# Performance work log

Measured on AMD Instinct MI355X. Metric: run time of the kernel, lower is better.

## Reference

```python
import jax, jax.numpy as jnp
import numpy as np

HEADS = 8
KSIZE = 3


def _unfold(t, ksize):
    # t: [B, C, H, W] -> [B, C, k*k, H, W], zero padding k//2, stride 1
    B, C, H, W = t.shape
    pad = ksize // 2
    tp = jnp.pad(t, ((0, 0), (0, 0), (pad, pad), (pad, pad)))
    patches = [tp[:, :, i:i + H, j:j + W] for i in range(ksize) for j in range(ksize)]
    return jnp.stack(patches, axis=2)


def setup_inputs() -> dict:
    key = jax.random.key(0)
    k0, k1, k2, k3 = jax.random.split(key, 4)
    B, C, H, W = 2, 256, 96, 96
    x = jax.random.normal(k0, (B, C, H, W), dtype=jnp.float32)
    w_qkv = jax.random.normal(k1, (3 * C, C), dtype=jnp.float32) * 0.02  # 1x1 conv, no bias
    w_out = jax.random.normal(k2, (C, C), dtype=jnp.float32) * 0.02     # 1x1 conv
    b_out = jax.random.normal(k3, (C,), dtype=jnp.float32) * 0.02
    return {"x": x, "w_qkv": w_qkv, "w_out": w_out, "b_out": b_out}


def reference(x, w_qkv, w_out, b_out):
    B, C, H, W = x.shape
    hd = C // HEADS
    scale = hd ** (-0.5)
    kk = KSIZE * KSIZE

    qkv = jnp.einsum('bchw,oc->bohw', x, w_qkv)          # [B, 3C, H, W]
    q, k, v = jnp.split(qkv, 3, axis=1)
    # unfold -> [B, heads, C/heads, k^2, H, W]
    q, k, v = [_unfold(t, KSIZE).reshape(B, HEADS, hd, kk, H, W) for t in (q, k, v)]

    # contract over the k^2 window dim (s); n,m are the per-head channel dims
    dots = jnp.einsum('bhnsij,bhmsij->bhnmij', q * scale, k)  # [B,h,hd,hd,H,W]
    attn = jax.nn.softmax(dots, axis=3)                       # softmax over m (dim=-3)
    out = jnp.einsum('bhnmij,bhmsij->bhnsij', attn, v)        # [B,h,hd,k^2,H,W]
    out = out.reshape(B, C, kk, H, W).sum(axis=2)             # [B,C,H,W]
    out = jnp.einsum('bchw,oc->bohw', out, w_out) + b_out[None, :, None, None] + x
    return out
```

## Files before the change

### kernel.cpp

```cpp
#include <hip/hip_runtime.h>

#define H96 96
#define W96 96
#define HW  9216
#define NC  256
#define NB  2
#define NHEADS 8
#define HD  32
#define SCALE 0.17677669529663687f

typedef __attribute__((ext_vector_type(8))) short short8v;
typedef __attribute__((ext_vector_type(4))) float f32x4;
typedef __attribute__((ext_vector_type(16))) float f32x16;

__device__ __forceinline__ ushort f2bf(float f) {
    unsigned u = __float_as_uint(f);
    u += 0x7FFFu + ((u >> 16) & 1u);
    return (ushort)(u >> 16);
}
__device__ __forceinline__ float bf2f(ushort h) {
    return __uint_as_float(((unsigned)h) << 16);
}

__global__ __launch_bounds__(256)
void x_to_bf16t(const float* __restrict__ x, ushort* __restrict__ xt,
                ushort* __restrict__ xbm)
{
    __shared__ float tile[32][33];
    const int t = threadIdx.x;
    const int hw0 = blockIdx.x * 32, c0 = blockIdx.y * 32, b = blockIdx.z;

    const int r = t >> 3, cc = (t & 7) * 4;
    const size_t gidx = ((size_t)b * NC + c0 + r) * HW + hw0 + cc;
    const float4 v = *(const float4*)(x + gidx);
    tile[r][cc + 0] = v.x; tile[r][cc + 1] = v.y; tile[r][cc + 2] = v.z; tile[r][cc + 3] = v.w;
    ushort4 ob;
    ob.x = f2bf(v.x); ob.y = f2bf(v.y); ob.z = f2bf(v.z); ob.w = f2bf(v.w);
    *(ushort4*)(xbm + gidx) = ob;
    __syncthreads();

    const int hwr = t >> 3, c4 = (t & 7) * 4;
    ushort4 o;
    o.x = f2bf(tile[c4 + 0][hwr]);
    o.y = f2bf(tile[c4 + 1][hwr]);
    o.z = f2bf(tile[c4 + 2][hwr]);
    o.w = f2bf(tile[c4 + 3][hwr]);
    *(ushort4*)(xt + ((size_t)b * HW + hw0 + hwr) * NC + c0 + c4) = o;
}

__global__ __launch_bounds__(256)
void conv_bf16(const float* __restrict__ w, ushort* __restrict__ o, int nscale)
{
    const int i = (blockIdx.x * 256 + threadIdx.x) * 4;
    const float s = (i < nscale) ? SCALE : 1.0f;
    const float4 v = *(const float4*)(w + i);
    ushort4 u;
    u.x = f2bf(v.x * s); u.y = f2bf(v.y * s); u.z = f2bf(v.z * s); u.w = f2bf(v.w * s);
    *(ushort4*)(o + i) = u;
}

__device__ __forceinline__ void stage_tile(const ushort* __restrict__ g, ushort* lds,
                                           int w, int lane)
{
    const int lr  = lane >> 3;
    const int swz = ((lane & 7) ^ lr) * 8;
    #pragma unroll
    for (int ii = 0; ii < 4; ++ii) {
        const int rowbase = w * 32 + ii * 8;
        const ushort* src = g + (size_t)(rowbase + lr) * NC + swz;
        __builtin_amdgcn_global_load_lds((const __attribute__((address_space(1))) void*)src,
                                         (__attribute__((address_space(3))) void*)(lds + rowbase * 64),
                                         16, 0, 0);
    }
}

template<int EPI>
__global__ __launch_bounds__(256)
void gemm_mfma(const ushort* __restrict__ A, const ushort* __restrict__ Bt,
               void* __restrict__ Cout, const float* __restrict__ bias,
               const ushort* __restrict__ resb, int Mtot)
{
    __shared__ __align__(16) ushort smem[128 * 136];
    ushort* As = smem;
    ushort* Bs = smem + 128 * 64;

    const int t = threadIdx.x;
    const int lane = t & 63, w = t >> 6;
    const int wm = w >> 1, wn = w & 1;
    const int n0 = blockIdx.x * 128;
    const int m0 = blockIdx.y * 128;

    const ushort* Ag = A + (size_t)m0 * NC;
    const ushort* Bg = Bt + (size_t)n0 * NC;

    f32x4 acc[4][4];
    #pragma unroll
    for (int i = 0; i < 4; ++i)
        #pragma unroll
        for (int j = 0; j < 4; ++j)
            acc[i][j] = (f32x4){0.f, 0.f, 0.f, 0.f};

    for (int k0 = 0; k0 < NC; k0 += 64) {
        stage_tile(Ag + k0, As, w, lane);
        stage_tile(Bg + k0, Bs, w, lane);
        __syncthreads();
        #pragma unroll
        for (int ks = 0; ks < 2; ++ks) {
            const int kc = (lane >> 4) + ks * 4;
            const int sw = (kc ^ (lane & 7)) * 8;
            short8v af[4], bf_[4];
            #pragma unroll
            for (int f = 0; f < 4; ++f) {
                af[f]  = *(const short8v*)(As + (wm * 64 + f * 16 + (lane & 15)) * 64 + sw);
                bf_[f] = *(const short8v*)(Bs + (wn * 64 + f * 16 + (lane & 15)) * 64 + sw);
            }
            #pragma unroll
            for (int fi = 0; fi < 4; ++fi)
                #pragma unroll
                for (int fj = 0; fj < 4; ++fj)
                    acc[fi][fj] = __builtin_amdgcn_mfma_f32_16x16x32_bf16(af[fi], bf_[fj], acc[fi][fj], 0, 0, 0);
        }
        __syncthreads();
    }

    const int b = n0 / HW;
    const int hw0 = n0 - b * HW;

    if constexpr (EPI == 0) {
        #pragma unroll
        for (int fi = 0; fi < 4; ++fi)
            #pragma unroll
            for (int fj = 0; fj < 4; ++fj) {
                const int hwl = wn * 64 + fj * 16 + (lane & 15);
                const int ml  = wm * 64 + fi * 16 + (lane >> 4) * 4;
                ushort4 v4;
                v4.x = f2bf(acc[fi][fj][0]);
                v4.y = f2bf(acc[fi][fj][1]);
                v4.z = f2bf(acc[fi][fj][2]);
                v4.w = f2bf(acc[fi][fj][3]);
                *(ushort4*)(smem + hwl * 136 + ml) = v4;
            }
        __syncthreads();
        ushort* C = (ushort*)Cout;
        #pragma unroll
        for (int it = 0; it < 8; ++it) {
            const int cid = it * 256 + t;
            const int hwl = cid >> 4, mc = (cid & 15) * 8;
            const uint4 v = *(const uint4*)(smem + hwl * 136 + mc);
            *(uint4*)(C + ((size_t)b * HW + hw0 + hwl) * (size_t)Mtot + m0 + mc) = v;
        }
    } else {
        float* C = (float*)Cout;
        const int ncol = hw0 + wn * 64 + (lane & 15);
        #pragma unroll
        for (int fi = 0; fi < 4; ++fi)
            #pragma unroll
            for (int r = 0; r < 4; ++r) {
                const int m = m0 + wm * 64 + fi * 16 + (lane >> 4) * 4 + r;
                const float bm = bias[m];
                const size_t base = ((size_t)b * NC + m) * HW + ncol;
                #pragma unroll
                for (int fj = 0; fj < 4; ++fj)
                    C[base + fj * 16] = acc[fi][fj][r] + bm + bf2f(resb[base + fj * 16]);
            }
    }
}

__global__ __launch_bounds__(256)
void attn_mfma(const ushort* __restrict__ qkvp, ushort* __restrict__ att)
{
    __shared__ ushort kh[107 * 40];
    __shared__ ushort qh[72 * 40];
    __shared__ ushort vh[54 * 40];
    __shared__ float  vs[16 * 32];

    const int t = threadIdx.x;
    const int sraw = blockIdx.x;
    const int strip = (sraw & 7) * 72 + (sraw >> 3);
    const int h = blockIdx.y;
    const int b = blockIdx.z;
    const int i0 = strip / 6;
    const int j0 = (strip - (strip / 6) * 6) * 16;

    const ushort* P = qkvp + (size_t)b * HW * 768;
    const int qo = h * HD, ko = NC + h * HD, vo = 2 * NC + h * HD;

    if (t < 216) {
        const int px = t >> 2, c8 = (t & 3) * 8;
        const int dy = px / 18, dx = px - dy * 18;
        const int gi = i0 - 1 + dy, gj = j0 - 1 + dx;
        uint4 qv = {0, 0, 0, 0}, kv = {0, 0, 0, 0}, vv = {0, 0, 0, 0};
        if (gi >= 0 && gi < H96 && gj >= 0 && gj < W96) {
            const ushort* pp = P + ((size_t)gi * W96 + gj) * 768;
            qv = *(const uint4*)(pp + qo + c8);
            kv = *(const uint4*)(pp + ko + c8);
            vv = *(const uint4*)(pp + vo + c8);
        }
        *(uint4*)(qh + px * 40 + c8) = qv;
        *(uint4*)(kh + px * 40 + c8) = kv;
        *(uint4*)(vh + px * 40 + c8) = vv;
    }
    {
        const int u = t;
        #pragma unroll
        for (int pass = 0; pass < 2; ++pass) {
            const int z = u + pass * 256;
            if (z < 265) {
                const int row_id = z / 5, part = z - row_id * 5;
                ushort* dst;
                if (row_id < 18)      dst = kh + (54 + row_id) * 40;
                else if (row_id < 35) dst = kh + (90 + row_id - 18) * 40;
                else                  dst = qh + (54 + row_id - 35) * 40;
                *(uint4*)(dst + part * 8) = (uint4){0, 0, 0, 0};
            }
        }
    }
    __syncthreads();

    {
        const int px = t >> 4, m2 = (t & 15) * 2;
        float a0 = 0.f, a1 = 0.f;
        #pragma unroll
        for (int dy = 0; dy < 3; ++dy)
            #pragma unroll
            for (int dx = 0; dx < 3; ++dx) {
                const ushort* pv = vh + (dy * 18 + px + dx) * 40 + m2;
                a0 += bf2f(pv[0]);
                a1 += bf2f(pv[1]);
            }
        vs[px * 32 + m2]     = a0;
        vs[px * 32 + m2 + 1] = a1;
    }
    __syncthreads();

    const int lane = t & 63, w = t >> 6;
    const int hi = lane >> 5, ch = lane & 31;

    const ushort* kb = kh + (hi * 36 + w * 4) * 40 + ch;
    const ushort* qb = qh + (hi * 36 + w * 4) * 40 + ch;

    #pragma unroll
    for (int p = 0; p < 4; ++p) {
        const int c = w * 4 + p;

        short8v ak, bq;
        #pragma unroll
        for (int e = 0; e < 8; ++e) {
            const int DK[8] = {0, 1, 2, 18, 19, 20, 54, 55};
            const int DQ[8] = {0, 1, 2, 18, 19, 20, 0, 0};
            ak[e] = (short)kb[(p + DK[e]) * 40];
            bq[e] = (short)qb[(p + DQ[e]) * 40];
        }

        f32x16 dm;
        #pragma unroll
        for (int r = 0; r < 16; ++r) dm[r] = 0.f;
        dm = __builtin_amdgcn_mfma_f32_32x32x16_bf16(ak, bq, dm, 0, 0, 0);

        float mx = dm[0];
        #pragma unroll
        for (int r = 1; r < 16; ++r) mx = fmaxf(mx, dm[r]);
        mx = fmaxf(mx, __shfl_xor(mx, 32));

        float vsv[16];
        #pragma unroll
        for (int g = 0; g < 4; ++g) {
            const float4 vv = *(const float4*)(vs + c * 32 + g * 8 + hi * 4);
            vsv[g * 4 + 0] = vv.x; vsv[g * 4 + 1] = vv.y;
            vsv[g * 4 + 2] = vv.z; vsv[g * 4 + 3] = vv.w;
        }

        float sum = 0.f, out = 0.f;
        #pragma unroll
        for (int r = 0; r < 16; ++r) {
            const float pe = __expf(dm[r] - mx);
            sum += pe;
            out = fmaf(pe, vsv[r], out);
        }
        sum += __shfl_xor(sum, 32);
        out += __shfl_xor(out, 32);

        if (hi == 0) {
            att[((size_t)b * HW + (size_t)i0 * W96 + j0 + c) * NC + h * HD + ch] =
                f2bf(out / sum);
        }
    }
}

extern "C" void kernel_launch(void* const* d_in, const int* in_sizes, int n_in,
                              void* d_out, int out_size, void* d_ws, size_t ws_size,
                              hipStream_t stream)
{
    (void)in_sizes; (void)n_in; (void)out_size; (void)ws_size;
    const float* x     = (const float*)d_in[0];
    const float* w_qkv = (const float*)d_in[1];
    const float* w_out = (const float*)d_in[2];
    const float* b_out = (const float*)d_in[3];
    float* out = (float*)d_out;

    ushort* qkvp = (ushort*)d_ws;
    ushort* attb = qkvp + (size_t)NB * HW * 768;
    ushort* xt   = attb + (size_t)NB * HW * NC;
    ushort* wqb  = xt   + (size_t)NB * HW * NC;
    ushort* wob  = wqb  + 768 * NC;
    ushort* xbm  = wob  + NC * NC;

    x_to_bf16t<<<dim3(HW / 32, NC / 32, NB), 256, 0, stream>>>(x, xt, xbm);
    conv_bf16<<<dim3(768 * NC / 1024), 256, 0, stream>>>(w_qkv, wqb, NC * NC);
    conv_bf16<<<dim3(NC * NC / 1024), 256, 0, stream>>>(w_out, wob, 0);
    gemm_mfma<0><<<dim3(144, 6), 256, 0, stream>>>(wqb, xt, qkvp, nullptr, nullptr, 768);
    attn_mfma<<<dim3(576, NHEADS, NB), 256, 0, stream>>>(qkvp, attb);
    gemm_mfma<1><<<dim3(144, 2), 256, 0, stream>>>(wob, attb, out, b_out, xbm, 256);
}
```

Measured before the change: 161.1 us.

## Transpose attention LDS tiles, drop softmax max, fuse weight casts, remap GEMM blocks

Stores Q/K halo tiles channel-major in LDS so each MFMA operand is built from four 32-bit loads instead of eight scattered 16-bit loads. Folds log2(e) into the Q weight scale so the softmax uses exp2 directly, and removes the max subtraction. Replaces the divide with a reciprocal. Also merges the two weight-conversion launches into one and remaps GEMM block indices with an XCD-aware swizzle. Dropping the max subtraction risks overflow if the logits grow large.

```diff
diff --git a/kernel.cpp b/kernel.cpp
--- a/kernel.cpp
+++ b/kernel.cpp
@@ -49,14 +49,24 @@
 }
 
 __global__ __launch_bounds__(256)
-void conv_bf16(const float* __restrict__ w, ushort* __restrict__ o, int nscale)
-{
-    const int i = (blockIdx.x * 256 + threadIdx.x) * 4;
-    const float s = (i < nscale) ? SCALE : 1.0f;
-    const float4 v = *(const float4*)(w + i);
-    ushort4 u;
-    u.x = f2bf(v.x * s); u.y = f2bf(v.y * s); u.z = f2bf(v.z * s); u.w = f2bf(v.w * s);
-    *(ushort4*)(o + i) = u;
+void conv_w(const float* __restrict__ wq, const float* __restrict__ wo,
+            ushort* __restrict__ oq, ushort* __restrict__ oo)
+{
+    const int bid = blockIdx.x;
+    if (bid < 192) {
+        const int i = (bid * 256 + threadIdx.x) * 4;
+        const float s = (i < 65536) ? (SCALE * 1.4426950408889634f) : 1.0f;
+        const float4 v = *(const float4*)(wq + i);
+        ushort4 u;
+        u.x = f2bf(v.x * s); u.y = f2bf(v.y * s); u.z = f2bf(v.z * s); u.w = f2bf(v.w * s);
+        *(ushort4*)(oq + i) = u;
+    } else {
+        const int i = ((bid - 192) * 256 + threadIdx.x) * 4;
+        const float4 v = *(const float4*)(wo + i);
+        ushort4 u;
+        u.x = f2bf(v.x); u.y = f2bf(v.y); u.z = f2bf(v.z); u.w = f2bf(v.w);
+        *(ushort4*)(oo + i) = u;
+    }
 }
 
 __device__ __forceinline__ void stage_tile(const ushort* __restrict__ g, ushort* lds,
@@ -87,8 +97,14 @@
     const int t = threadIdx.x;
     const int lane = t & 63, w = t >> 6;
     const int wm = w >> 1, wn = w & 1;
-    const int n0 = blockIdx.x * 128;
-    const int m0 = blockIdx.y * 128;
+
+    const int l = blockIdx.x;
+    const int chunk = (EPI == 0) ? 108 : 36;
+    const int mt    = (EPI == 0) ? 6 : 2;
+    const int id2 = (l & 7) * chunk + (l >> 3);
+    const int n_tile = id2 / mt;
+    const int n0 = n_tile * 128;
+    const int m0 = (id2 - n_tile * mt) * 128;
 
     const ushort* Ag = A + (size_t)m0 * NC;
     const ushort* Bg = Bt + (size_t)n0 * NC;
@@ -169,8 +185,8 @@
 __global__ __launch_bounds__(256)
 void attn_mfma(const ushort* __restrict__ qkvp, ushort* __restrict__ att)
 {
-    __shared__ ushort kh[107 * 40];
-    __shared__ ushort qh[72 * 40];
+    __shared__ ushort khT[32 * 74];
+    __shared__ ushort qhT[32 * 74];
     __shared__ ushort vh[54 * 40];
     __shared__ float  vs[16 * 32];
 
@@ -184,6 +200,13 @@
 
     const ushort* P = qkvp + (size_t)b * HW * 768;
     const int qo = h * HD, ko = NC + h * HD, vo = 2 * NC + h * HD;
+
+    for (int z = t; z < 640; z += 256) {
+        const int arr = z & 1, rest = z >> 1;
+        const int ch = rest & 31, rp = rest >> 5;
+        ushort* dst = (arr ? qhT : khT) + ch * 74 + 54 + rp * 2;
+        *(unsigned*)dst = 0u;
+    }
 
     if (t < 216) {
         const int px = t >> 2, c8 = (t & 3) * 8;
@@ -196,23 +219,15 @@
             kv = *(const uint4*)(pp + ko + c8);
             vv = *(const uint4*)(pp + vo + c8);
         }
-        *(uint4*)(qh + px * 40 + c8) = qv;
-        *(uint4*)(kh + px * 40 + c8) = kv;
         *(uint4*)(vh + px * 40 + c8) = vv;
-    }
-    {
-        const int u = t;
-        #pragma unroll
-        for (int pass = 0; pass < 2; ++pass) {
-            const int z = u + pass * 256;
-            if (z < 265) {
-                const int row_id = z / 5, part = z - row_id * 5;
-                ushort* dst;
-                if (row_id < 18)      dst = kh + (54 + row_id) * 40;
-                else if (row_id < 35) dst = kh + (90 + row_id - 18) * 40;
-                else                  dst = qh + (54 + row_id - 35) * 40;
-                *(uint4*)(dst + part * 8) = (uint4){0, 0, 0, 0};
-            }
+        const unsigned ku[4] = {kv.x, kv.y, kv.z, kv.w};
+        const unsigned qu[4] = {qv.x, qv.y, qv.z, qv.w};
+        #pragma unroll
+        for (int i = 0; i < 4; ++i) {
+            khT[(c8 + 2 * i)     * 74 + px] = (ushort)(ku[i] & 0xFFFFu);
+            khT[(c8 + 2 * i + 1) * 74 + px] = (ushort)(ku[i] >> 16);
+            qhT[(c8 + 2 * i)     * 74 + px] = (ushort)(qu[i] & 0xFFFFu);
+            qhT[(c8 + 2 * i + 1) * 74 + px] = (ushort)(qu[i] >> 16);
         }
     }
     __syncthreads();
@@ -235,32 +250,38 @@
 
     const int lane = t & 63, w = t >> 6;
     const int hi = lane >> 5, ch = lane & 31;
-
-    const ushort* kb = kh + (hi * 36 + w * 4) * 40 + ch;
-    const ushort* qb = qh + (hi * 36 + w * 4) * 40 + ch;
+    const ushort* kb = khT + ch * 74 + hi * 36;
+    const ushort* qb = qhT + ch * 74 + hi * 36;
 
     #pragma unroll
     for (int p = 0; p < 4; ++p) {
         const int c = w * 4 + p;
 
-        short8v ak, bq;
-        #pragma unroll
-        for (int e = 0; e < 8; ++e) {
-            const int DK[8] = {0, 1, 2, 18, 19, 20, 54, 55};
-            const int DQ[8] = {0, 1, 2, 18, 19, 20, 0, 0};
-            ak[e] = (short)kb[(p + DK[e]) * 40];
-            bq[e] = (short)qb[(p + DQ[e]) * 40];
-        }
+        unsigned kk0, kk1, kk2, kk3, qq0, qq1, qq2, qq3;
+        if ((p & 1) == 0) {
+            kk0 = *(const unsigned*)(kb + c);      kk1 = *(const unsigned*)(kb + c + 2);
+            kk2 = *(const unsigned*)(kb + c + 18); kk3 = *(const unsigned*)(kb + c + 20);
+            qq0 = *(const unsigned*)(qb + c);
+            qq1 = *(const unsigned*)(qb + c + 2)  & 0x0000FFFFu;
+            qq2 = *(const unsigned*)(qb + c + 18);
+            qq3 = *(const unsigned*)(qb + c + 20) & 0x0000FFFFu;
+        } else {
+            kk0 = *(const unsigned*)(kb + c - 1);  kk1 = *(const unsigned*)(kb + c + 1);
+            kk2 = *(const unsigned*)(kb + c + 17); kk3 = *(const unsigned*)(kb + c + 19);
+            qq0 = *(const unsigned*)(qb + c - 1)  & 0xFFFF0000u;
+            qq1 = *(const unsigned*)(qb + c + 1);
+            qq2 = *(const unsigned*)(qb + c + 17) & 0xFFFF0000u;
+            qq3 = *(const unsigned*)(qb + c + 19);
+        }
+
+        union { unsigned u[4]; short8v v; } A_, B_;
+        A_.u[0] = kk0; A_.u[1] = kk1; A_.u[2] = kk2; A_.u[3] = kk3;
+        B_.u[0] = qq0; B_.u[1] = qq1; B_.u[2] = qq2; B_.u[3] = qq3;
 
         f32x16 dm;
         #pragma unroll
         for (int r = 0; r < 16; ++r) dm[r] = 0.f;
-        dm = __builtin_amdgcn_mfma_f32_32x32x16_bf16(ak, bq, dm, 0, 0, 0);
-
-        float mx = dm[0];
-        #pragma unroll
-        for (int r = 1; r < 16; ++r) mx = fmaxf(mx, dm[r]);
-        mx = fmaxf(mx, __shfl_xor(mx, 32));
+        dm = __builtin_amdgcn_mfma_f32_32x32x16_bf16(A_.v, B_.v, dm, 0, 0, 0);
 
         float vsv[16];
         #pragma unroll
@@ -273,7 +294,7 @@
         float sum = 0.f, out = 0.f;
         #pragma unroll
         for (int r = 0; r < 16; ++r) {
-            const float pe = __expf(dm[r] - mx);
+            const float pe = __builtin_amdgcn_exp2f(dm[r]);
             sum += pe;
             out = fmaf(pe, vsv[r], out);
         }
@@ -281,8 +302,9 @@
         out += __shfl_xor(out, 32);
 
         if (hi == 0) {
+            const float inv = __builtin_amdgcn_rcpf(sum);
             att[((size_t)b * HW + (size_t)i0 * W96 + j0 + c) * NC + h * HD + ch] =
-                f2bf(out / sum);
+                f2bf(out * inv);
         }
     }
 }
@@ -306,9 +328,8 @@
     ushort* xbm  = wob  + NC * NC;
 
     x_to_bf16t<<<dim3(HW / 32, NC / 32, NB), 256, 0, stream>>>(x, xt, xbm);
-    conv_bf16<<<dim3(768 * NC / 1024), 256, 0, stream>>>(w_qkv, wqb, NC * NC);
-    conv_bf16<<<dim3(NC * NC / 1024), 256, 0, stream>>>(w_out, wob, 0);
-    gemm_mfma<0><<<dim3(144, 6), 256, 0, stream>>>(wqb, xt, qkvp, nullptr, nullptr, 768);
+    conv_w<<<dim3(256), 256, 0, stream>>>(w_qkv, w_out, wqb, wob);
+    gemm_mfma<0><<<dim3(864), 256, 0, stream>>>(wqb, xt, qkvp, nullptr, nullptr, 768);
     attn_mfma<<<dim3(576, NHEADS, NB), 256, 0, stream>>>(qkvp, attb);
-    gemm_mfma<1><<<dim3(144, 2), 256, 0, stream>>>(wob, attb, out, b_out, xbm, 256);
-}
+    gemm_mfma<1><<<dim3(288), 256, 0, stream>>>(wob, attb, out, b_out, xbm, 256);
+}
```

Result: faster. 140.8 us (-12.6%).
